# Optimization experiments

Measured on AMD Instinct MI355X. Metric: run time of the kernel, lower is better.

Reference implementation:

```python
import jax, jax.numpy as jnp
import numpy as np

N_HEADS = 8
D_HEAD = 64  # n_embd=512 / n_heads=8


def setup_inputs() -> dict:
    key = jax.random.key(0)
    ks = jax.random.split(key, 5)
    B, T, C = 2, 4096, 512
    x = jax.random.normal(ks[0], (B, T, C), dtype=jnp.float32)
    s = 1.0 / np.sqrt(C)
    Wq = jax.random.normal(ks[1], (C, C), dtype=jnp.float32) * s
    Wk = jax.random.normal(ks[2], (C, C), dtype=jnp.float32) * s
    Wv = jax.random.normal(ks[3], (C, C), dtype=jnp.float32) * s
    Wout = jax.random.normal(ks[4], (C, C), dtype=jnp.float32) * s
    return {"x": x, "Wq": Wq, "Wk": Wk, "Wv": Wv, "Wout": Wout}


def reference(x, Wq, Wk, Wv, Wout):
    # x: [B,T,C]; nn.Linear(y) = y @ W.T, here weights stored as [C,C] used directly
    B, T, C = x.shape
    H, D = N_HEADS, D_HEAD
    q = (x @ Wq.T).reshape(B, T, H, D).transpose(0, 2, 1, 3)  # [B,H,T,D]
    k = (x @ Wk.T).reshape(B, T, H, D).transpose(0, 2, 1, 3)
    v = (x @ Wv.T).reshape(B, T, H, D).transpose(0, 2, 1, 3)
    att = jnp.einsum('bhqd,bhkd->bhqk', q, k) / jnp.sqrt(jnp.float32(D))  # [B,H,T,T]
    causal = jnp.tril(jnp.ones((T, T), dtype=bool))
    att = jnp.where(causal, att, -jnp.inf)
    att = jax.nn.softmax(att, axis=-1)
    # dropout is identity in eval mode (p=0)
    y = jnp.einsum('bhqk,bhkd->bhqd', att, v)  # [B,H,T,D]
    y = y.transpose(0, 2, 1, 3).reshape(B, T, C)
    return y @ Wout.T
```

## Files before the change

kernel.cpp:

```cpp
#include <hip/hip_runtime.h>
#include <hip/hip_bf16.h>
#include <math.h>
#include <stdint.h>

using bf16 = __hip_bfloat16;
typedef __attribute__((ext_vector_type(8))) short short8;
typedef __attribute__((ext_vector_type(4))) short short4v;
typedef __attribute__((ext_vector_type(4))) float float4v;

#define MFMA16(a, b, c) __builtin_amdgcn_mfma_f32_16x16x32_bf16(a, b, c, 0, 0, 0)

__device__ __forceinline__ short bfbits(float f) {
  bf16 h = (bf16)f;
  return *(short*)&h;
}

__device__ __forceinline__ short8 ld_cvt8(const float* p) {
  union { float4v v[2]; float f[8]; } u;
  u.v[0] = *(const float4v*)p;
  u.v[1] = *(const float4v*)(p + 4);
  short8 r;
#pragma unroll
  for (int j = 0; j < 8; j++) r[j] = bfbits(u.f[j]);
  return r;
}

__global__ __launch_bounds__(256) void conv_all(
    const float* __restrict__ x, const float* __restrict__ w0,
    const float* __restrict__ w1, const float* __restrict__ w2,
    const float* __restrict__ w3, bf16* __restrict__ cx,
    bf16* __restrict__ cw) {
  size_t gid = ((size_t)blockIdx.x * 256 + threadIdx.x) * 8;
  const float* src;
  bf16* dst;
  size_t off;
  if (gid < 4194304) {
    src = x; dst = cx; off = gid;
  } else {
    size_t r = gid - 4194304;
    int wi = (int)(r >> 18);
    src = wi == 0 ? w0 : wi == 1 ? w1 : wi == 2 ? w2 : w3;
    dst = cw + ((size_t)wi << 18);
    off = r & 262143;
  }
  *(short8*)(dst + off) = ld_cvt8(src + off);
}

template <int MODE, int MT>
__device__ __forceinline__ void gemm_body(bf16* As, bf16* Bs,
                                          const bf16* __restrict__ A,
                                          const bf16* __restrict__ W,
                                          void* __restrict__ outp,
                                          float oscale) {
  constexpr int STR = 40;
  constexpr int MI = MT / 32;
  const int bm = blockIdx.x * MT, bn = blockIdx.y * 128;
  const int tid = threadIdx.x;
  const int lane = tid & 63;
  const int wave = tid >> 6;
  const int lr = lane & 15, quad = lane >> 4;
  const int wm = (wave & 1) * (MT / 2), wn = (wave >> 1) * 64;

  const int lrow = tid >> 2;
  const int lcol = (tid & 3) * 8;
  const bf16* a0 = A + (size_t)(bm + lrow) * 512 + lcol;
  const bf16* a1 = a0 + (size_t)64 * 512;
  const bf16* b0 = W + (size_t)(bn + lrow) * 512 + lcol;
  const bf16* b1 = b0 + (size_t)64 * 512;
  bf16* as0 = &As[lrow * STR + lcol];
  bf16* as1 = &As[(lrow + 64) * STR + lcol];
  bf16* bs0 = &Bs[lrow * STR + lcol];
  bf16* bs1 = &Bs[(lrow + 64) * STR + lcol];

  short8 ra0, ra1, rb0, rb1;
  ra0 = *(const short8*)a0;
  if (MT == 128) ra1 = *(const short8*)a1;
  rb0 = *(const short8*)b0;
  rb1 = *(const short8*)b1;

  float4v acc[MI][4] = {};

  for (int k0 = 0; k0 < 512; k0 += 32) {
    __syncthreads();
    *(short8*)as0 = ra0;
    if (MT == 128) *(short8*)as1 = ra1;
    *(short8*)bs0 = rb0;
    *(short8*)bs1 = rb1;
    __syncthreads();
    if (k0 + 32 < 512) {
      ra0 = *(const short8*)(a0 + k0 + 32);
      if (MT == 128) ra1 = *(const short8*)(a1 + k0 + 32);
      rb0 = *(const short8*)(b0 + k0 + 32);
      rb1 = *(const short8*)(b1 + k0 + 32);
    }
    short8 af[MI], bfv[4];
#pragma unroll
    for (int i = 0; i < MI; i++)
      af[i] = *(const short8*)&As[(wm + i * 16 + lr) * STR + quad * 8];
#pragma unroll
    for (int i = 0; i < 4; i++)
      bfv[i] = *(const short8*)&Bs[(wn + i * 16 + lr) * STR + quad * 8];
#pragma unroll
    for (int mi = 0; mi < MI; mi++)
#pragma unroll
      for (int ni = 0; ni < 4; ni++)
        acc[mi][ni] = MFMA16(af[mi], bfv[ni], acc[mi][ni]);
  }

  const int row0 = bm + wm + quad * 4;
  const int col0 = bn + wn + lr;
#pragma unroll
  for (int mi = 0; mi < MI; mi++) {
#pragma unroll
    for (int ni = 0; ni < 4; ni++) {
      const int col = col0 + ni * 16;
      if (MODE == 1) {
        float* out = (float*)outp;
#pragma unroll
        for (int i = 0; i < 4; i++) {
          int m = row0 + mi * 16 + i;
          out[(size_t)m * 512 + col] = acc[mi][ni][i];
        }
      } else if (MODE == 0) {
        bf16* out = (bf16*)outp;
        const int hh = col >> 6, d = col & 63;
#pragma unroll
        for (int i = 0; i < 4; i++) {
          int m = row0 + mi * 16 + i;
          int bb = m >> 12, t = m & 4095;
          out[(((size_t)(bb * 8 + hh) * 4096 + t) << 6) + d] =
              (bf16)(acc[mi][ni][i] * oscale);
        }
      } else {
        bf16* out = (bf16*)outp;
        const int hh = col >> 6, d = col & 63;
        int m0 = row0 + mi * 16;
        int bb = m0 >> 12, t0 = m0 & 4095;
        short4v pk;
#pragma unroll
        for (int i = 0; i < 4; i++) pk[i] = bfbits(acc[mi][ni][i]);
        *(short4v*)&out[(((size_t)(bb * 8 + hh) * 64 + d) << 12) + t0] = pk;
      }
    }
  }
}

#define QSCALE 0.18033688f

__global__ __launch_bounds__(256) void qkv_kernel(
    const bf16* __restrict__ cx, const bf16* __restrict__ cW,
    bf16* q, bf16* k, bf16* vt) {
  __shared__ __align__(16) bf16 As[128 * 40];
  __shared__ __align__(16) bf16 Bs[128 * 40];
  if (blockIdx.z == 0)      gemm_body<0, 128>(As, Bs, cx, cW, q, QSCALE);
  else if (blockIdx.z == 1) gemm_body<0, 128>(As, Bs, cx, cW + 262144, k, 1.0f);
  else                      gemm_body<2, 128>(As, Bs, cx, cW + 2 * 262144, vt, 1.0f);
}

__global__ __launch_bounds__(256) void proj_kernel(
    const bf16* __restrict__ y, const bf16* __restrict__ cWout,
    float* __restrict__ out) {
  __shared__ __align__(16) bf16 As[64 * 40];
  __shared__ __align__(16) bf16 Bs[128 * 40];
  gemm_body<1, 64>(As, Bs, y, cWout, out, 1.0f);
}

__device__ __forceinline__ int lsw(int row, int col) {
  return (row << 6) + (col ^ ((row & 7) << 3));
}

template <bool DIAG>
__device__ __forceinline__ void attn_step(const bf16* __restrict__ Kc,
                                          const bf16* __restrict__ Vc,
                                          short8 qf0, short8 qf1,
                                          int wave, int lr, int quad,
                                          float& l_i, float4v* O) {
  float4v S[4] = {};
#pragma unroll
  for (int nc = 0; nc < 4; nc++) {
    short8 kf0 = *(const short8*)&Kc[lsw(nc * 16 + lr, quad * 8)];
    short8 kf1 = *(const short8*)&Kc[lsw(nc * 16 + lr, 32 + quad * 8)];
    S[nc] = MFMA16(kf0, qf0, S[nc]);
    S[nc] = MFMA16(kf1, qf1, S[nc]);
  }

  short8 pf0, pf1;
#pragma unroll
  for (int nc = 0; nc < 4; nc++) {
#pragma unroll
    for (int i = 0; i < 4; i++) {
      float pv = exp2f(S[nc][i]);
      if (DIAG) {
        int kl = nc * 16 + quad * 4 + i;
        pv = (kl > wave * 16 + lr) ? 0.f : pv;
      }
      l_i += pv;
      short bb = bfbits(pv);
      if (nc == 0)      pf0[i] = bb;
      else if (nc == 1) pf0[4 + i] = bb;
      else if (nc == 2) pf1[i] = bb;
      else              pf1[4 + i] = bb;
    }
  }

#pragma unroll
  for (int nc = 0; nc < 4; nc++) {
    const int row = nc * 16 + lr;
    short4v va0 = *(const short4v*)&Vc[lsw(row, 4 * quad)];
    short4v va1 = *(const short4v*)&Vc[lsw(row, 16 + 4 * quad)];
    short4v vb0 = *(const short4v*)&Vc[lsw(row, 32 + 4 * quad)];
    short4v vb1 = *(const short4v*)&Vc[lsw(row, 48 + 4 * quad)];
    short8 vfa, vfb;
#pragma unroll
    for (int j = 0; j < 4; j++) {
      vfa[j] = va0[j]; vfa[4 + j] = va1[j];
      vfb[j] = vb0[j]; vfb[4 + j] = vb1[j];
    }
    O[nc] = MFMA16(pf0, vfa, O[nc]);
    O[nc] = MFMA16(pf1, vfb, O[nc]);
  }
}

__global__ __launch_bounds__(256, 4) void attn_kernel(const bf16* __restrict__ Qg,
                                                      const bf16* __restrict__ Kg,
                                                      const bf16* __restrict__ Vtg,
                                                      bf16* __restrict__ Y) {
  constexpr int T = 4096;
  __shared__ __align__(16) bf16 Ks[2][64 * 64];
  __shared__ __align__(16) bf16 Vts[2][64 * 64];

  const int bx = blockIdx.x;
  const int g = bx >> 8, r = bx & 255;
  const int a = r >> 4, hb = r & 15;
  const int qt = (g == 0) ? a : (g == 1) ? 16 + a : (g == 2) ? 63 - a : 47 - a;
  const int h = hb >> 1, b = hb & 1;
  const size_t ho = ((size_t)(b * 8 + h)) * T * 64;
  const bf16* Qh = Qg + ho;
  const bf16* Kh = Kg + ho;
  const bf16* Vth = Vtg + ho;

  const int tid = threadIdx.x;
  const int wave = tid >> 6, lane = tid & 63;
  const int lr = lane & 15, quad = lane >> 4;

  const int sr = tid >> 3;
  const int sc = (tid & 7) * 8;
  const bf16* ksrc0 = Kh + (size_t)sr * 64 + sc;
  const bf16* ksrc1 = ksrc0 + 32 * 64;
  const bf16* vsrc0 = Vth + (size_t)sr * T + sc;
  const bf16* vsrc1 = vsrc0 + (size_t)32 * T;
  const int d0 = lsw(sr, sc);
  const int d1 = lsw(sr + 32, sc);

  short8 rk0 = *(const short8*)ksrc0;
  short8 rk1 = *(const short8*)ksrc1;
  short8 rv0 = *(const short8*)vsrc0;
  short8 rv1 = *(const short8*)vsrc1;

  short8 qf0, qf1;
  for (int s = tid; s < 512; s += 256) {
    int rr = s >> 3, c = (s & 7) * 8;
    *(short8*)&Ks[1][lsw(rr, c)] =
        *(const short8*)&Qh[(size_t)(qt * 64 + rr) * 64 + c];
  }
  __syncthreads();
  qf0 = *(const short8*)&Ks[1][lsw(wave * 16 + lr, quad * 8)];
  qf1 = *(const short8*)&Ks[1][lsw(wave * 16 + lr, 32 + quad * 8)];
  *(short8*)&Ks[0][d0] = rk0;
  *(short8*)&Ks[0][d1] = rk1;
  *(short8*)&Vts[0][d0] = rv0;
  *(short8*)&Vts[0][d1] = rv1;
  __syncthreads();

  float l_i = 0.f;
  float4v O[4] = {};

  for (int kt = 0; kt < qt; kt++) {
    const int cur = kt & 1, nxt = cur ^ 1;
    {
      const size_t ko = (size_t)(kt + 1) * 4096;
      const size_t vo = (size_t)(kt + 1) * 64;
      rk0 = *(const short8*)(ksrc0 + ko);
      rk1 = *(const short8*)(ksrc1 + ko);
      rv0 = *(const short8*)(vsrc0 + vo);
      rv1 = *(const short8*)(vsrc1 + vo);
    }

    attn_step<false>(Ks[cur], Vts[cur], qf0, qf1, wave, lr, quad, l_i, O);

    *(short8*)&Ks[nxt][d0] = rk0;
    *(short8*)&Ks[nxt][d1] = rk1;
    *(short8*)&Vts[nxt][d0] = rv0;
    *(short8*)&Vts[nxt][d1] = rv1;
    __syncthreads();
  }
  attn_step<true>(Ks[qt & 1], Vts[qt & 1], qf0, qf1, wave, lr, quad, l_i, O);

  l_i += __shfl_xor(l_i, 16, 64);
  l_i += __shfl_xor(l_i, 32, 64);
  const float linv = 1.f / l_i;
  float lrow[4];
#pragma unroll
  for (int i = 0; i < 4; i++) lrow[i] = __shfl(linv, quad * 4 + i, 64);

  const size_t yb = ((size_t)b * T + qt * 64 + wave * 16 + quad * 4) * 512 + h * 64;
#pragma unroll
  for (int nc = 0; nc < 4; nc++)
#pragma unroll
    for (int i = 0; i < 4; i++)
      Y[yb + (size_t)i * 512 + nc * 16 + lr] = (bf16)(O[nc][i] * lrow[i]);
}

extern "C" void kernel_launch(void* const* d_in, const int* in_sizes, int n_in,
                              void* d_out, int out_size, void* d_ws, size_t ws_size,
                              hipStream_t stream) {
  (void)out_size; (void)ws_size;
  const int NX = 8192 * 512;
  int xi = 0;
  for (int i = 0; i < n_in; i++)
    if (in_sizes[i] == NX) { xi = i; break; }
  const float* x = (const float*)d_in[xi];
  const float* wsrc[4];
  int wn = 0;
  for (int i = 0; i < n_in && wn < 4; i++)
    if (i != xi) wsrc[wn++] = (const float*)d_in[i];

  bf16* ws = (bf16*)d_ws;
  const size_t HE = (size_t)NX;
  bf16* q  = ws;
  bf16* k  = q + HE;
  bf16* yx = k + HE;
  bf16* cw = yx + HE;
  bf16* vt = (bf16*)d_out;
  float* out = (float*)d_out;

  conv_all<<<2560, 256, 0, stream>>>(x, wsrc[0], wsrc[1], wsrc[2], wsrc[3],
                                     yx, cw);
  qkv_kernel<<<dim3(64, 4, 3), 256, 0, stream>>>(yx, cw, q, k, vt);
  attn_kernel<<<1024, 256, 0, stream>>>(q, k, vt, yx);
  proj_kernel<<<dim3(128, 4), 256, 0, stream>>>(yx, cw + 3 * 262144, out);
}
```

Measured before the change: 188.1 us.

## Load GEMM tiles directly into LDS with swizzled layout and K-step 64

```diff
diff --git a/kernel.cpp b/kernel.cpp
--- a/kernel.cpp
+++ b/kernel.cpp
@@ -23,6 +23,12 @@
 #pragma unroll
   for (int j = 0; j < 8; j++) r[j] = bfbits(u.f[j]);
   return r;
+}
+
+__device__ __forceinline__ void gload16(const bf16* g, bf16* l) {
+  __builtin_amdgcn_global_load_lds(
+      (const __attribute__((address_space(1))) void*)g,
+      (__attribute__((address_space(3))) void*)l, 16, 0, 0);
 }
 
 __global__ __launch_bounds__(256) void conv_all(
@@ -52,7 +58,6 @@
                                           const bf16* __restrict__ W,
                                           void* __restrict__ outp,
                                           float oscale) {
-  constexpr int STR = 40;
   constexpr int MI = MT / 32;
   const int bm = blockIdx.x * MT, bn = blockIdx.y * 128;
   const int tid = threadIdx.x;
@@ -61,50 +66,44 @@
   const int lr = lane & 15, quad = lane >> 4;
   const int wm = (wave & 1) * (MT / 2), wn = (wave >> 1) * 64;
 
-  const int lrow = tid >> 2;
-  const int lcol = (tid & 3) * 8;
-  const bf16* a0 = A + (size_t)(bm + lrow) * 512 + lcol;
-  const bf16* a1 = a0 + (size_t)64 * 512;
-  const bf16* b0 = W + (size_t)(bn + lrow) * 512 + lcol;
-  const bf16* b1 = b0 + (size_t)64 * 512;
-  bf16* as0 = &As[lrow * STR + lcol];
-  bf16* as1 = &As[(lrow + 64) * STR + lcol];
-  bf16* bs0 = &Bs[lrow * STR + lcol];
-  bf16* bs1 = &Bs[(lrow + 64) * STR + lcol];
-
-  short8 ra0, ra1, rb0, rb1;
-  ra0 = *(const short8*)a0;
-  if (MT == 128) ra1 = *(const short8*)a1;
-  rb0 = *(const short8*)b0;
-  rb1 = *(const short8*)b1;
+  const int srow = lane >> 3;
+  const int scl = (lane & 7) ^ (srow & 7);
+  const int rsw = lr & 7;
 
   float4v acc[MI][4] = {};
 
-  for (int k0 = 0; k0 < 512; k0 += 32) {
+  for (int k0 = 0; k0 < 512; k0 += 64) {
     __syncthreads();
-    *(short8*)as0 = ra0;
-    if (MT == 128) *(short8*)as1 = ra1;
-    *(short8*)bs0 = rb0;
-    *(short8*)bs1 = rb1;
+#pragma unroll
+    for (int j = 0; j < MT / 32; j++) {
+      const int m = wave + 4 * j;
+      gload16(&A[(size_t)(bm + 8 * m + srow) * 512 + k0 + scl * 8],
+              &As[(8 * m) * 64]);
+    }
+#pragma unroll
+    for (int j = 0; j < 4; j++) {
+      const int m = wave + 4 * j;
+      gload16(&W[(size_t)(bn + 8 * m + srow) * 512 + k0 + scl * 8],
+              &Bs[(8 * m) * 64]);
+    }
     __syncthreads();
-    if (k0 + 32 < 512) {
-      ra0 = *(const short8*)(a0 + k0 + 32);
-      if (MT == 128) ra1 = *(const short8*)(a1 + k0 + 32);
-      rb0 = *(const short8*)(b0 + k0 + 32);
-      rb1 = *(const short8*)(b1 + k0 + 32);
-    }
-    short8 af[MI], bfv[4];
-#pragma unroll
-    for (int i = 0; i < MI; i++)
-      af[i] = *(const short8*)&As[(wm + i * 16 + lr) * STR + quad * 8];
-#pragma unroll
-    for (int i = 0; i < 4; i++)
-      bfv[i] = *(const short8*)&Bs[(wn + i * 16 + lr) * STR + quad * 8];
-#pragma unroll
-    for (int mi = 0; mi < MI; mi++)
-#pragma unroll
-      for (int ni = 0; ni < 4; ni++)
-        acc[mi][ni] = MFMA16(af[mi], bfv[ni], acc[mi][ni]);
+#pragma unroll
+    for (int kk = 0; kk < 2; kk++) {
+      short8 af[MI], bfv[4];
+#pragma unroll
+      for (int i = 0; i < MI; i++)
+        af[i] = *(const short8*)
+            &As[(wm + i * 16 + lr) * 64 + ((4 * kk + quad) ^ rsw) * 8];
+#pragma unroll
+      for (int i = 0; i < 4; i++)
+        bfv[i] = *(const short8*)
+            &Bs[(wn + i * 16 + lr) * 64 + ((4 * kk + quad) ^ rsw) * 8];
+#pragma unroll
+      for (int mi = 0; mi < MI; mi++)
+#pragma unroll
+        for (int ni = 0; ni < 4; ni++)
+          acc[mi][ni] = MFMA16(af[mi], bfv[ni], acc[mi][ni]);
+    }
   }
 
   const int row0 = bm + wm + quad * 4;
@@ -150,8 +149,8 @@
 __global__ __launch_bounds__(256) void qkv_kernel(
     const bf16* __restrict__ cx, const bf16* __restrict__ cW,
     bf16* q, bf16* k, bf16* vt) {
-  __shared__ __align__(16) bf16 As[128 * 40];
-  __shared__ __align__(16) bf16 Bs[128 * 40];
+  __shared__ __align__(16) bf16 As[128 * 64];
+  __shared__ __align__(16) bf16 Bs[128 * 64];
   if (blockIdx.z == 0)      gemm_body<0, 128>(As, Bs, cx, cW, q, QSCALE);
   else if (blockIdx.z == 1) gemm_body<0, 128>(As, Bs, cx, cW + 262144, k, 1.0f);
   else                      gemm_body<2, 128>(As, Bs, cx, cW + 2 * 262144, vt, 1.0f);
@@ -160,8 +159,8 @@
 __global__ __launch_bounds__(256) void proj_kernel(
     const bf16* __restrict__ y, const bf16* __restrict__ cWout,
     float* __restrict__ out) {
-  __shared__ __align__(16) bf16 As[64 * 40];
-  __shared__ __align__(16) bf16 Bs[128 * 40];
+  __shared__ __align__(16) bf16 As[64 * 64];
+  __shared__ __align__(16) bf16 Bs[128 * 64];
   gemm_body<1, 64>(As, Bs, y, cWout, out, 1.0f);
 }
 
```

Result: faster. 179.0 us (-4.8%).
